# Optimization experiments

Measured on AMD Instinct MI355X. Metric: run time of the kernel, lower is better.

Reference implementation:

```python
import jax, jax.numpy as jnp
import numpy as np

N_NODES = 50000
N_EDGES = 1600000
D_EDGE = 32
D_NODE = 32
D_HID = 128
D_OUT = 32


def setup_inputs() -> dict:
    key = jax.random.key(0)
    ks = jax.random.split(key, 8)
    edge_feats = jax.random.normal(ks[0], (N_EDGES, D_EDGE), dtype=jnp.float32)
    node_feats = jax.random.normal(ks[1], (N_NODES, D_NODE), dtype=jnp.float32)
    senders = jax.random.randint(ks[2], (N_EDGES,), 0, N_NODES, dtype=jnp.int64 if jax.config.jax_enable_x64 else jnp.int32)
    receivers = jax.random.randint(ks[3], (N_EDGES,), 0, N_NODES, dtype=jnp.int64 if jax.config.jax_enable_x64 else jnp.int32)
    d_in = D_EDGE + 2 * D_NODE  # 96
    W1 = jax.random.normal(ks[4], (d_in, D_HID), dtype=jnp.float32) / jnp.sqrt(jnp.float32(d_in))
    b1 = jnp.zeros((D_HID,), dtype=jnp.float32)
    W2 = jax.random.normal(ks[5], (D_HID, D_OUT), dtype=jnp.float32) / jnp.sqrt(jnp.float32(D_HID))
    b2 = jnp.zeros((D_OUT,), dtype=jnp.float32)
    return {"edge_feats": edge_feats, "node_feats": node_feats, "senders": senders,
            "receivers": receivers, "W1": W1, "b1": b1, "W2": W2, "b2": b2}


def reference(edge_feats, node_feats, senders, receivers, W1, b1, W2, b2):
    # Gather node feats to edges (target=0 -> senders, target=1 -> receivers),
    # concat with edge feats along feature dim, then edge MLP.
    sender_feats = node_feats[senders]        # [E, D_NODE]
    receiver_feats = node_feats[receivers]    # [E, D_NODE]
    collected = jnp.concatenate([edge_feats, sender_feats, receiver_feats], axis=1)  # [E, 96]
    h = jax.nn.relu(collected @ W1 + b1)      # [E, 128]
    updated_edges = h @ W2 + b2               # [E, 32]
    return updated_edges
```

## Files before the change

kernel.cpp:

```cpp
#include <hip/hip_runtime.h>

typedef __attribute__((ext_vector_type(8))) short bf16x8;
typedef __attribute__((ext_vector_type(4))) float f32x4;
typedef unsigned short ushort_t;
typedef unsigned int uint32;

#define TILE 64
#define N_EDGES 1600000
#define NT (N_EDGES / TILE)
#define GRID 512

#define CSTR 104
#define HSTR 136
#define W1_US (128 * CSTR)
#define W2_US (32 * HSTR)
#define WEIGHT_US (W1_US + W2_US)
#define WBUF (16 * HSTR)
#define SMEM_USHORTS WEIGHT_US

__device__ __forceinline__ ushort_t f2bf(float x) {
    uint32 u = __builtin_bit_cast(uint32, x);
    u += 0x7FFFu + ((u >> 16) & 1u);
    return (ushort_t)(u >> 16);
}
__device__ __forceinline__ uint32 pack2(float a, float b) {
    return (uint32)f2bf(a) | ((uint32)f2bf(b) << 16);
}
__device__ __forceinline__ void store_bf16x8(ushort_t* dst, f32x4 a, f32x4 b) {
    uint4 p;
    p.x = pack2(a[0], a[1]);
    p.y = pack2(a[2], a[3]);
    p.z = pack2(b[0], b[1]);
    p.w = pack2(b[2], b[3]);
    *reinterpret_cast<uint4*>(dst) = p;
}

__global__ __launch_bounds__(256, 2)
void edge_mlp_kernel(const float* __restrict__ edge_feats,
                     const float* __restrict__ node_feats,
                     const int* __restrict__ senders,
                     const int* __restrict__ receivers,
                     const float* __restrict__ W1,
                     const float* __restrict__ b1,
                     const float* __restrict__ W2,
                     const float* __restrict__ b2,
                     float* __restrict__ out)
{
    __shared__ __align__(16) ushort_t smem[SMEM_USHORTS];

    const int tid = threadIdx.x;
    const int l   = tid & 63;
    const int llo = l & 15;
    const int lhi = l >> 4;
    const int w   = tid >> 6;
    const int r   = l >> 2;
    const int q   = l & 3;

    {
        ushort_t* w1t = smem;
        ushort_t* w2t = smem + W1_US;
        for (int idx = tid; idx < 96 * 128; idx += 256) {
            int k = idx >> 7, n = idx & 127;
            w1t[n * CSTR + k] = f2bf(W1[idx]);
        }
        for (int idx = tid; idx < 128 * 32; idx += 256) {
            int n = idx >> 5, o = idx & 31;
            w2t[o * HSTR + n] = f2bf(W2[idx]);
        }
    }
    __syncthreads();

    bf16x8 w1f[8][3];
#pragma unroll
    for (int ni = 0; ni < 8; ++ni)
#pragma unroll
        for (int kk = 0; kk < 3; ++kk)
            w1f[ni][kk] = *reinterpret_cast<const bf16x8*>(
                smem + (ni * 16 + llo) * CSTR + kk * 32 + lhi * 8);
    bf16x8 w2f[2][4];
#pragma unroll
    for (int oi = 0; oi < 2; ++oi)
#pragma unroll
        for (int kk = 0; kk < 4; ++kk)
            w2f[oi][kk] = *reinterpret_cast<const bf16x8*>(
                smem + W1_US + (oi * 16 + llo) * HSTR + kk * 32 + lhi * 8);

    f32x4 b1v[8], b2v[2];
#pragma unroll
    for (int ni = 0; ni < 8; ++ni)
        b1v[ni] = *reinterpret_cast<const f32x4*>(b1 + ni * 16 + lhi * 4);
#pragma unroll
    for (int oi = 0; oi < 2; ++oi)
        b2v[oi] = *reinterpret_cast<const f32x4*>(b2 + oi * 16 + lhi * 4);

    __syncthreads();

    ushort_t* buf = smem + w * WBUF;

    const long stride = gridDim.x;
    const long last = (long)NT - 1;
    long t = blockIdx.x;

    long eS = t * TILE + w * 16 + r;
    int si_c = senders[eS], ri_c = receivers[eS];
    f32x4 ea, eb, sa, sb, ra, rb;
    {
        const f32x4* efp = reinterpret_cast<const f32x4*>(edge_feats + eS * 32) + q * 2;
        ea = efp[0]; eb = efp[1];
        const f32x4* sp = reinterpret_cast<const f32x4*>(node_feats + (long)si_c * 32) + q * 2;
        sa = sp[0]; sb = sp[1];
        const f32x4* rp = reinterpret_cast<const f32x4*>(node_feats + (long)ri_c * 32) + q * 2;
        ra = rp[0]; rb = rp[1];
    }
    long ts1 = t + stride; ts1 = ts1 <= last ? ts1 : last;
    long eS1 = ts1 * TILE + w * 16 + r;
    int si_n = senders[eS1], ri_n = receivers[eS1];

    for (; t < NT; t += stride) {
        ushort_t* cw = buf + r * CSTR + q * 8;
        store_bf16x8(cw,      ea, eb);
        store_bf16x8(cw + 32, sa, sb);
        store_bf16x8(cw + 64, ra, rb);

        long tn = t + stride; tn = tn <= last ? tn : last;
        {
            long eN = tn * TILE + w * 16 + r;
            const f32x4* efp = reinterpret_cast<const f32x4*>(edge_feats + eN * 32) + q * 2;
            ea = efp[0]; eb = efp[1];
            const f32x4* sp = reinterpret_cast<const f32x4*>(node_feats + (long)si_n * 32) + q * 2;
            sa = sp[0]; sb = sp[1];
            const f32x4* rp = reinterpret_cast<const f32x4*>(node_feats + (long)ri_n * 32) + q * 2;
            ra = rp[0]; rb = rp[1];
        }
        long tn2 = t + 2 * stride; tn2 = tn2 <= last ? tn2 : last;
        long eN2 = tn2 * TILE + w * 16 + r;
        si_n = senders[eN2]; ri_n = receivers[eN2];

        f32x4 acc1[8];
#pragma unroll
        for (int ni = 0; ni < 8; ++ni) acc1[ni] = b1v[ni];
        const ushort_t* crow = buf + llo * CSTR + lhi * 8;
        __builtin_amdgcn_s_setprio(1);
#pragma unroll
        for (int kk = 0; kk < 3; ++kk) {
            bf16x8 bfrag = *reinterpret_cast<const bf16x8*>(crow + kk * 32);
#pragma unroll
            for (int ni = 0; ni < 8; ++ni)
                acc1[ni] = __builtin_amdgcn_mfma_f32_16x16x32_bf16(w1f[ni][kk], bfrag, acc1[ni], 0, 0, 0);
        }
        __builtin_amdgcn_s_setprio(0);

#pragma unroll
        for (int ni = 0; ni < 8; ++ni) {
            float h0 = fmaxf(acc1[ni][0], 0.f);
            float h1 = fmaxf(acc1[ni][1], 0.f);
            float h2 = fmaxf(acc1[ni][2], 0.f);
            float h3 = fmaxf(acc1[ni][3], 0.f);
            uint2 p;
            p.x = pack2(h0, h1);
            p.y = pack2(h2, h3);
            *reinterpret_cast<uint2*>(buf + llo * HSTR + ni * 16 + lhi * 4) = p;
        }

        f32x4 acc2[2];
        acc2[0] = b2v[0];
        acc2[1] = b2v[1];
        const ushort_t* hrow = buf + llo * HSTR + lhi * 8;
        __builtin_amdgcn_s_setprio(1);
#pragma unroll
        for (int kk = 0; kk < 4; ++kk) {
            bf16x8 bfrag = *reinterpret_cast<const bf16x8*>(hrow + kk * 32);
#pragma unroll
            for (int oi = 0; oi < 2; ++oi)
                acc2[oi] = __builtin_amdgcn_mfma_f32_16x16x32_bf16(w2f[oi][kk], bfrag, acc2[oi], 0, 0, 0);
        }
        __builtin_amdgcn_s_setprio(0);

        float* orow = out + (t * TILE + w * 16 + llo) * 32 + lhi * 4;
        *reinterpret_cast<f32x4*>(orow)      = acc2[0];
        *reinterpret_cast<f32x4*>(orow + 16) = acc2[1];
    }
}

extern "C" void kernel_launch(void* const* d_in, const int* in_sizes, int n_in,
                              void* d_out, int out_size, void* d_ws, size_t ws_size,
                              hipStream_t stream) {
    const float* edge_feats = (const float*)d_in[0];
    const float* node_feats = (const float*)d_in[1];
    const int*   senders    = (const int*)d_in[2];
    const int*   receivers  = (const int*)d_in[3];
    const float* W1         = (const float*)d_in[4];
    const float* b1         = (const float*)d_in[5];
    const float* W2         = (const float*)d_in[6];
    const float* b2         = (const float*)d_in[7];
    float* out = (float*)d_out;

    dim3 grid(GRID), block(256);
    hipLaunchKernelGGL(edge_mlp_kernel, grid, block, 0, stream,
                       edge_feats, node_feats, senders, receivers, W1, b1, W2, b2, out);
}
```

Baseline: 381.8 us.

## Keep most of W1 in LDS to cut registers and raise occupancy

Only the first K-slice of W1 fragments stays in registers. The other two slices are re-read from LDS on every tile, which frees VGPRs so launch bounds can go from 2 to 3 blocks per CU and the grid from 512 to 768 blocks. Per-wave scratch buffers move past the persistent W1 region and overlap the W2 staging area. Software bf16 rounding is replaced by the v_cvt_pk_bf16_f32 instruction, and index math moves from 64-bit to 32-bit ints. The trade is extra LDS read traffic and bank pressure per tile in exchange for more waves in flight to hide gather latency.

New measurement: 468.6 us. 1.23x slower.

```diff
diff --git a/kernel.cpp b/kernel.cpp
--- a/kernel.cpp
+++ b/kernel.cpp
@@ -8,34 +8,34 @@
 #define TILE 64
 #define N_EDGES 1600000
 #define NT (N_EDGES / TILE)
-#define GRID 512
+#define GRID 768
 
 #define CSTR 104
 #define HSTR 136
 #define W1_US (128 * CSTR)
-#define W2_US (32 * HSTR)
-#define WEIGHT_US (W1_US + W2_US)
 #define WBUF (16 * HSTR)
-#define SMEM_USHORTS WEIGHT_US
+#define SMEM_USHORTS (W1_US + 4 * WBUF)
 
 __device__ __forceinline__ ushort_t f2bf(float x) {
     uint32 u = __builtin_bit_cast(uint32, x);
     u += 0x7FFFu + ((u >> 16) & 1u);
     return (ushort_t)(u >> 16);
 }
-__device__ __forceinline__ uint32 pack2(float a, float b) {
-    return (uint32)f2bf(a) | ((uint32)f2bf(b) << 16);
+__device__ __forceinline__ uint32 cvt_pk_bf16(float lo, float hi) {
+    uint32 r;
+    asm("v_cvt_pk_bf16_f32 %0, %1, %2" : "=v"(r) : "v"(lo), "v"(hi));
+    return r;
 }
 __device__ __forceinline__ void store_bf16x8(ushort_t* dst, f32x4 a, f32x4 b) {
     uint4 p;
-    p.x = pack2(a[0], a[1]);
-    p.y = pack2(a[2], a[3]);
-    p.z = pack2(b[0], b[1]);
-    p.w = pack2(b[2], b[3]);
+    p.x = cvt_pk_bf16(a[0], a[1]);
+    p.y = cvt_pk_bf16(a[2], a[3]);
+    p.z = cvt_pk_bf16(b[0], b[1]);
+    p.w = cvt_pk_bf16(b[2], b[3]);
     *reinterpret_cast<uint4*>(dst) = p;
 }
 
-__global__ __launch_bounds__(256, 2)
+__global__ __launch_bounds__(256, 3)
 void edge_mlp_kernel(const float* __restrict__ edge_feats,
                      const float* __restrict__ node_feats,
                      const int* __restrict__ senders,
@@ -47,6 +47,7 @@
                      float* __restrict__ out)
 {
     __shared__ __align__(16) ushort_t smem[SMEM_USHORTS];
+    ushort_t* w1t = smem;
 
     const int tid = threadIdx.x;
     const int l   = tid & 63;
@@ -57,7 +58,6 @@
     const int q   = l & 3;
 
     {
-        ushort_t* w1t = smem;
         ushort_t* w2t = smem + W1_US;
         for (int idx = tid; idx < 96 * 128; idx += 256) {
             int k = idx >> 7, n = idx & 127;
@@ -70,13 +70,11 @@
     }
     __syncthreads();
 
-    bf16x8 w1f[8][3];
+    bf16x8 w1f0[8];
 #pragma unroll
     for (int ni = 0; ni < 8; ++ni)
-#pragma unroll
-        for (int kk = 0; kk < 3; ++kk)
-            w1f[ni][kk] = *reinterpret_cast<const bf16x8*>(
-                smem + (ni * 16 + llo) * CSTR + kk * 32 + lhi * 8);
+        w1f0[ni] = *reinterpret_cast<const bf16x8*>(
+            smem + (ni * 16 + llo) * CSTR + lhi * 8);
     bf16x8 w2f[2][4];
 #pragma unroll
     for (int oi = 0; oi < 2; ++oi)
@@ -95,25 +93,25 @@
 
     __syncthreads();
 
-    ushort_t* buf = smem + w * WBUF;
-
-    const long stride = gridDim.x;
-    const long last = (long)NT - 1;
-    long t = blockIdx.x;
-
-    long eS = t * TILE + w * 16 + r;
+    ushort_t* buf = smem + W1_US + w * WBUF;
+
+    const int stride = gridDim.x;
+    const int last = NT - 1;
+    int t = blockIdx.x;
+
+    int eS = t * TILE + w * 16 + r;
     int si_c = senders[eS], ri_c = receivers[eS];
     f32x4 ea, eb, sa, sb, ra, rb;
     {
-        const f32x4* efp = reinterpret_cast<const f32x4*>(edge_feats + eS * 32) + q * 2;
+        const f32x4* efp = reinterpret_cast<const f32x4*>(edge_feats + (size_t)eS * 32) + q * 2;
         ea = efp[0]; eb = efp[1];
-        const f32x4* sp = reinterpret_cast<const f32x4*>(node_feats + (long)si_c * 32) + q * 2;
+        const f32x4* sp = reinterpret_cast<const f32x4*>(node_feats + (size_t)si_c * 32) + q * 2;
         sa = sp[0]; sb = sp[1];
-        const f32x4* rp = reinterpret_cast<const f32x4*>(node_feats + (long)ri_c * 32) + q * 2;
+        const f32x4* rp = reinterpret_cast<const f32x4*>(node_feats + (size_t)ri_c * 32) + q * 2;
         ra = rp[0]; rb = rp[1];
     }
-    long ts1 = t + stride; ts1 = ts1 <= last ? ts1 : last;
-    long eS1 = ts1 * TILE + w * 16 + r;
+    int ts1 = t + stride; ts1 = ts1 <= last ? ts1 : last;
+    int eS1 = ts1 * TILE + w * 16 + r;
     int si_n = senders[eS1], ri_n = receivers[eS1];
 
     for (; t < NT; t += stride) {
@@ -122,43 +120,49 @@
         store_bf16x8(cw + 32, sa, sb);
         store_bf16x8(cw + 64, ra, rb);
 
-        long tn = t + stride; tn = tn <= last ? tn : last;
+        int tn = t + stride; tn = tn <= last ? tn : last;
         {
-            long eN = tn * TILE + w * 16 + r;
-            const f32x4* efp = reinterpret_cast<const f32x4*>(edge_feats + eN * 32) + q * 2;
+            int eN = tn * TILE + w * 16 + r;
+            const f32x4* efp = reinterpret_cast<const f32x4*>(edge_feats + (size_t)eN * 32) + q * 2;
             ea = efp[0]; eb = efp[1];
-            const f32x4* sp = reinterpret_cast<const f32x4*>(node_feats + (long)si_n * 32) + q * 2;
+            const f32x4* sp = reinterpret_cast<const f32x4*>(node_feats + (size_t)si_n * 32) + q * 2;
             sa = sp[0]; sb = sp[1];
-            const f32x4* rp = reinterpret_cast<const f32x4*>(node_feats + (long)ri_n * 32) + q * 2;
+            const f32x4* rp = reinterpret_cast<const f32x4*>(node_feats + (size_t)ri_n * 32) + q * 2;
             ra = rp[0]; rb = rp[1];
         }
-        long tn2 = t + 2 * stride; tn2 = tn2 <= last ? tn2 : last;
-        long eN2 = tn2 * TILE + w * 16 + r;
+        int tn2 = t + 2 * stride; tn2 = tn2 <= last ? tn2 : last;
+        int eN2 = tn2 * TILE + w * 16 + r;
         si_n = senders[eN2]; ri_n = receivers[eN2];
 
         f32x4 acc1[8];
 #pragma unroll
         for (int ni = 0; ni < 8; ++ni) acc1[ni] = b1v[ni];
         const ushort_t* crow = buf + llo * CSTR + lhi * 8;
+        const ushort_t* w1r  = w1t + llo * CSTR + lhi * 8;
+        bf16x8 bc0 = *reinterpret_cast<const bf16x8*>(crow);
+        bf16x8 bc1 = *reinterpret_cast<const bf16x8*>(crow + 32);
+        bf16x8 bc2 = *reinterpret_cast<const bf16x8*>(crow + 64);
         __builtin_amdgcn_s_setprio(1);
 #pragma unroll
-        for (int kk = 0; kk < 3; ++kk) {
-            bf16x8 bfrag = *reinterpret_cast<const bf16x8*>(crow + kk * 32);
-#pragma unroll
-            for (int ni = 0; ni < 8; ++ni)
-                acc1[ni] = __builtin_amdgcn_mfma_f32_16x16x32_bf16(w1f[ni][kk], bfrag, acc1[ni], 0, 0, 0);
+        for (int ni = 0; ni < 8; ++ni)
+            acc1[ni] = __builtin_amdgcn_mfma_f32_16x16x32_bf16(w1f0[ni], bc0, acc1[ni], 0, 0, 0);
+#pragma unroll
+        for (int ni = 0; ni < 8; ++ni) {
+            bf16x8 afrag = *reinterpret_cast<const bf16x8*>(w1r + ni * 16 * CSTR + 32);
+            acc1[ni] = __builtin_amdgcn_mfma_f32_16x16x32_bf16(afrag, bc1, acc1[ni], 0, 0, 0);
+        }
+#pragma unroll
+        for (int ni = 0; ni < 8; ++ni) {
+            bf16x8 afrag = *reinterpret_cast<const bf16x8*>(w1r + ni * 16 * CSTR + 64);
+            acc1[ni] = __builtin_amdgcn_mfma_f32_16x16x32_bf16(afrag, bc2, acc1[ni], 0, 0, 0);
         }
         __builtin_amdgcn_s_setprio(0);
 
 #pragma unroll
         for (int ni = 0; ni < 8; ++ni) {
-            float h0 = fmaxf(acc1[ni][0], 0.f);
-            float h1 = fmaxf(acc1[ni][1], 0.f);
-            float h2 = fmaxf(acc1[ni][2], 0.f);
-            float h3 = fmaxf(acc1[ni][3], 0.f);
             uint2 p;
-            p.x = pack2(h0, h1);
-            p.y = pack2(h2, h3);
+            p.x = cvt_pk_bf16(fmaxf(acc1[ni][0], 0.f), fmaxf(acc1[ni][1], 0.f));
+            p.y = cvt_pk_bf16(fmaxf(acc1[ni][2], 0.f), fmaxf(acc1[ni][3], 0.f));
             *reinterpret_cast<uint2*>(buf + llo * HSTR + ni * 16 + lhi * 4) = p;
         }
 
@@ -176,7 +180,7 @@
         }
         __builtin_amdgcn_s_setprio(0);
 
-        float* orow = out + (t * TILE + w * 16 + llo) * 32 + lhi * 4;
+        float* orow = out + (size_t)(t * TILE + w * 16 + llo) * 32 + lhi * 4;
         *reinterpret_cast<f32x4*>(orow)      = acc2[0];
         *reinterpret_cast<f32x4*>(orow + 16) = acc2[1];
     }
```
